# Kernel tuning notes

Measured on AMD Instinct MI355X. Metric: run time of the kernel, lower is better.

## Reference

```python
import jax, jax.numpy as jnp
import numpy as np

B, T, C, H = 4, 2048, 1024, 16
D = C // H  # head_size = 64


def setup_inputs() -> dict:
    key = jax.random.key(0)
    k1, k2, k3 = jax.random.split(key, 3)
    x = jax.random.normal(k1, (B, T, C), dtype=jnp.float32)
    w_qkv = jax.random.normal(k2, (C, 3 * C), dtype=jnp.float32) * (C ** -0.5)
    b_qkv = jnp.zeros((3 * C,), dtype=jnp.float32)
    w_proj = jax.random.normal(k3, (C, C), dtype=jnp.float32) * (C ** -0.5)
    b_proj = jnp.zeros((C,), dtype=jnp.float32)
    return {"x": x, "w_qkv": w_qkv, "b_qkv": b_qkv, "w_proj": w_proj, "b_proj": b_proj}


def reference(x, w_qkv, b_qkv, w_proj, b_proj):
    b, t, c = x.shape
    qkv = x @ w_qkv + b_qkv                      # [B,T,3C]
    q, k, v = jnp.split(qkv, 3, axis=-1)
    # [B,T,C] -> [B,H,T,D]
    q = q.reshape(b, t, H, D).transpose(0, 2, 1, 3)
    k = k.reshape(b, t, H, D).transpose(0, 2, 1, 3)
    v = v.reshape(b, t, H, D).transpose(0, 2, 1, 3)
    attn = jnp.einsum('bhqd,bhkd->bhqk', q, k) * (D ** -0.5)
    causal = jnp.tril(jnp.ones((t, t), dtype=bool))
    attn = jnp.where(causal[None, None], attn, -jnp.inf)
    attn = jax.nn.softmax(attn, axis=-1)
    # dropout: eval mode (identity)
    out = jnp.einsum('bhqk,bhkd->bhqd', attn, v)
    out = out.transpose(0, 2, 1, 3).reshape(b, t, c)
    return out @ w_proj + b_proj
```

## Files before the change

### kernel.cpp

```cpp
#include <hip/hip_runtime.h>

#define B_ 4
#define T_ 2048
#define C_ 1024
#define H_ 16
#define D_ 64

typedef __attribute__((ext_vector_type(8))) short short8;
typedef __attribute__((ext_vector_type(4))) float f32x4;

__device__ inline unsigned short f2bf(float f) {
    union { float f; unsigned u; } v; v.f = f;
    unsigned r = v.u + 0x7fffu + ((v.u >> 16) & 1u);
    return (unsigned short)(r >> 16);
}

__device__ inline unsigned int pk_bf16(float a, float b) {
#if __has_builtin(__builtin_amdgcn_cvt_pk_bf16_f32)
    typedef __attribute__((ext_vector_type(2))) __bf16 bf16x2;
    bf16x2 v = __builtin_amdgcn_cvt_pk_bf16_f32(a, b);
    return __builtin_bit_cast(unsigned int, v);
#else
    return (unsigned)f2bf(a) | ((unsigned)f2bf(b) << 16);
#endif
}

__device__ inline float dpp_max16(float x) {
    int t;
    t = __builtin_amdgcn_update_dpp(0, __builtin_bit_cast(int, x), 0xB1, 0xF, 0xF, true);
    x = fmaxf(x, __builtin_bit_cast(float, t));
    t = __builtin_amdgcn_update_dpp(0, __builtin_bit_cast(int, x), 0x4E, 0xF, 0xF, true);
    x = fmaxf(x, __builtin_bit_cast(float, t));
    t = __builtin_amdgcn_update_dpp(0, __builtin_bit_cast(int, x), 0x141, 0xF, 0xF, true);
    x = fmaxf(x, __builtin_bit_cast(float, t));
    t = __builtin_amdgcn_update_dpp(0, __builtin_bit_cast(int, x), 0x140, 0xF, 0xF, true);
    x = fmaxf(x, __builtin_bit_cast(float, t));
    return x;
}

__device__ inline void async_ld16(const void* g, void* lds) {
    __builtin_amdgcn_global_load_lds(
        (const __attribute__((address_space(1))) unsigned int*)g,
        (__attribute__((address_space(3))) unsigned int*)lds, 16, 0, 0);
}

__global__ __launch_bounds__(256) void prep_all(
    const float* __restrict__ x, const float* __restrict__ w_qkv,
    const float* __restrict__ w_proj,
    unsigned short* __restrict__ xb, unsigned short* __restrict__ wqkvT,
    unsigned short* __restrict__ wprojT)
{
    const int bid = blockIdx.x;
    if (bid < 8192) {
        int i = (bid * 256 + threadIdx.x) * 4;
        float4 v = *(const float4*)(x + i);
        uint2 o;
        o.x = pk_bf16(v.x, v.y);
        o.y = pk_bf16(v.z, v.w);
        *(uint2*)(xb + i) = o;
        return;
    }
    __shared__ float tile[32][33];
    const int tt = bid - 8192;
    int bx = tt & 127;
    const int by = tt >> 7;
    const float* src; unsigned short* dst; int Cc;
    if (bx < 96) { src = w_qkv;  dst = wqkvT;  Cc = 3072; }
    else         { src = w_proj; dst = wprojT; Cc = 1024; bx -= 96; }
    const int tx = threadIdx.x & 31, ty = threadIdx.x >> 5;
    #pragma unroll
    for (int r = 0; r < 32; r += 8)
        tile[ty + r][tx] = src[(size_t)(by*32 + ty + r) * Cc + bx*32 + tx];
    __syncthreads();
    #pragma unroll
    for (int r = 0; r < 32; r += 8)
        dst[(size_t)(bx*32 + ty + r) * 1024 + by*32 + tx] = f2bf(tile[tx][ty + r]);
}

__global__ __launch_bounds__(256) void gemm_qkv(
    const unsigned short* __restrict__ A,
    const unsigned short* __restrict__ BT,
    const float* __restrict__ bias,
    unsigned short* __restrict__ qb, unsigned short* __restrict__ kb,
    unsigned short* __restrict__ vtb)
{
    __shared__ unsigned short As0[128 * 32], As1[128 * 32];
    __shared__ unsigned short Bs0[128 * 32], Bs1[128 * 32];
    const int tid = threadIdx.x;
    const int wave = tid >> 6, lane = tid & 63;
    const int wm = wave >> 1, wn = wave & 1;
    const int l15 = lane & 15, lq = lane >> 4;
    const int m0 = blockIdx.y * 128, n0 = blockIdx.x * 128;
    const int srow = tid >> 2, sg = tid & 3;
    const int sel = n0 >> 10;

    f32x4 acc[4][4] = {};

    for (int k0 = 0; k0 < 1024; k0 += 64) {
        #pragma unroll
        for (int r = 0; r < 2; ++r) {
            const size_t ra = (size_t)(m0 + r*64 + srow) * 1024 + k0 + sg*8;
            const size_t rb = (size_t)(n0 + r*64 + srow) * 1024 + k0 + sg*8;
            async_ld16(A  + ra,      (char*)As0 + r*4096 + wave*1024);
            async_ld16(A  + ra + 32, (char*)As1 + r*4096 + wave*1024);
            async_ld16(BT + rb,      (char*)Bs0 + r*4096 + wave*1024);
            async_ld16(BT + rb + 32, (char*)Bs1 + r*4096 + wave*1024);
        }
        __syncthreads();
        #pragma unroll
        for (int ks = 0; ks < 2; ++ks) {
            const unsigned short* Asx = ks ? As1 : As0;
            const unsigned short* Bsx = ks ? Bs1 : Bs0;
            short8 af[4], bf[4];
            #pragma unroll
            for (int i = 0; i < 4; ++i) {
                af[i] = *(const short8*)&Asx[(wm*64 + i*16 + l15) * 32 + lq*8];
                bf[i] = *(const short8*)&Bsx[(wn*64 + i*16 + l15) * 32 + lq*8];
            }
            if (sel < 2) {
                #pragma unroll
                for (int mi = 0; mi < 4; ++mi)
                    #pragma unroll
                    for (int ni = 0; ni < 4; ++ni)
                        acc[mi][ni] = __builtin_amdgcn_mfma_f32_16x16x32_bf16(
                            bf[ni], af[mi], acc[mi][ni], 0, 0, 0);
            } else {
                #pragma unroll
                for (int mi = 0; mi < 4; ++mi)
                    #pragma unroll
                    for (int ni = 0; ni < 4; ++ni)
                        acc[mi][ni] = __builtin_amdgcn_mfma_f32_16x16x32_bf16(
                            af[mi], bf[ni], acc[mi][ni], 0, 0, 0);
            }
        }
        __syncthreads();
    }

    if (sel < 2) {
        const float qs = (sel == 0) ? 0.180336880f : 1.0f;
        unsigned short* dst = (sel == 0) ? qb : kb;
        #pragma unroll
        for (int mi = 0; mi < 4; ++mi) {
            const int t = m0 + wm*64 + mi*16 + l15;
            const int bb = t >> 11, tt = t & 2047;
            #pragma unroll
            for (int ni = 0; ni < 4; ++ni) {
                const int nb = n0 + wn*64 + ni*16 + lq*4;
                const int hh = (nb >> 6) & 15, d0 = nb & 63;
                float4 bv = *(const float4*)(bias + nb);
                float v0 = (acc[mi][ni][0] + bv.x) * qs;
                float v1 = (acc[mi][ni][1] + bv.y) * qs;
                float v2 = (acc[mi][ni][2] + bv.z) * qs;
                float v3 = (acc[mi][ni][3] + bv.w) * qs;
                uint2 pk; pk.x = pk_bf16(v0, v1); pk.y = pk_bf16(v2, v3);
                *(uint2*)(dst + ((size_t)(bb*16 + hh)*2048 + tt)*64 + d0) = pk;
            }
        }
    } else {
        #pragma unroll
        for (int mi = 0; mi < 4; ++mi) {
            const int t0 = m0 + wm*64 + mi*16 + lq*4;
            const int bb = t0 >> 11, tt = t0 & 2047;
            #pragma unroll
            for (int ni = 0; ni < 4; ++ni) {
                const int n = n0 + wn*64 + ni*16 + l15;
                const int hh = (n >> 6) & 15, d = n & 63;
                const float bs = bias[n];
                uint2 pk;
                pk.x = pk_bf16(acc[mi][ni][0] + bs, acc[mi][ni][1] + bs);
                pk.y = pk_bf16(acc[mi][ni][2] + bs, acc[mi][ni][3] + bs);
                *(uint2*)(vtb + ((size_t)(bb*16 + hh)*64 + d)*2048 + tt) = pk;
            }
        }
    }
}

__global__ __launch_bounds__(256) void gemm_proj(
    const unsigned short* __restrict__ A,
    const unsigned short* __restrict__ BT,
    const float* __restrict__ bias,
    float* __restrict__ out)
{
    __shared__ unsigned short As0[128 * 32], As1[128 * 32];
    __shared__ unsigned short Bs0[128 * 32], Bs1[128 * 32];
    const int tid = threadIdx.x;
    const int wave = tid >> 6, lane = tid & 63;
    const int wm = wave >> 1, wn = wave & 1;
    const int l15 = lane & 15, lq = lane >> 4;
    const int m0 = blockIdx.y * 128, n0 = blockIdx.x * 128;
    const int srow = tid >> 2, sg = tid & 3;

    f32x4 acc[4][4] = {};

    for (int k0 = 0; k0 < 1024; k0 += 64) {
        #pragma unroll
        for (int r = 0; r < 2; ++r) {
            const size_t ra = (size_t)(m0 + r*64 + srow) * 1024 + k0 + sg*8;
            const size_t rb = (size_t)(n0 + r*64 + srow) * 1024 + k0 + sg*8;
            async_ld16(A  + ra,      (char*)As0 + r*4096 + wave*1024);
            async_ld16(A  + ra + 32, (char*)As1 + r*4096 + wave*1024);
            async_ld16(BT + rb,      (char*)Bs0 + r*4096 + wave*1024);
            async_ld16(BT + rb + 32, (char*)Bs1 + r*4096 + wave*1024);
        }
        __syncthreads();
        #pragma unroll
        for (int ks = 0; ks < 2; ++ks) {
            const unsigned short* Asx = ks ? As1 : As0;
            const unsigned short* Bsx = ks ? Bs1 : Bs0;
            short8 af[4], bf[4];
            #pragma unroll
            for (int i = 0; i < 4; ++i) {
                af[i] = *(const short8*)&Asx[(wm*64 + i*16 + l15) * 32 + lq*8];
                bf[i] = *(const short8*)&Bsx[(wn*64 + i*16 + l15) * 32 + lq*8];
            }
            #pragma unroll
            for (int mi = 0; mi < 4; ++mi)
                #pragma unroll
                for (int ni = 0; ni < 4; ++ni)
                    acc[mi][ni] = __builtin_amdgcn_mfma_f32_16x16x32_bf16(
                        bf[ni], af[mi], acc[mi][ni], 0, 0, 0);
        }
        __syncthreads();
    }

    #pragma unroll
    for (int mi = 0; mi < 4; ++mi) {
        const int m = m0 + wm*64 + mi*16 + l15;
        #pragma unroll
        for (int ni = 0; ni < 4; ++ni) {
            const int nb = n0 + wn*64 + ni*16 + lq*4;
            float4 bv = *(const float4*)(bias + nb);
            float4 o;
            o.x = acc[mi][ni][0] + bv.x;
            o.y = acc[mi][ni][1] + bv.y;
            o.z = acc[mi][ni][2] + bv.z;
            o.w = acc[mi][ni][3] + bv.w;
            *(float4*)(out + (size_t)m * 1024 + nb) = o;
        }
    }
}

__global__ __launch_bounds__(256, 5) void attn_mfma(
    const unsigned short* __restrict__ qb,
    const unsigned short* __restrict__ kb,
    const unsigned short* __restrict__ vtb,
    unsigned short* __restrict__ ab)
{
    __shared__ unsigned short Ks[64][72];
    __shared__ unsigned short Vt[80][72];
    __shared__ unsigned short Ps[64][72];

    const int tid  = threadIdx.x;
    const int wave = tid >> 6, lane = tid & 63;
    const int l15  = lane & 15, lq = lane >> 4;
    const int linear = blockIdx.x;
    const int xc  = linear & 7;
    const int idx = linear >> 3;
    const int bh  = xc * 8 + (idx & 7);
    const int qblk = 31 - (idx >> 3);
    const int q0 = qblk * 64;
    const int b = bh >> 4, h = bh & 15;
    const size_t base = (size_t)bh * 2048 * 64;

    for (int i = tid; i < 16 * 72; i += 256) {
        int r = i / 72, cc = i - r * 72;
        Vt[64 + r][cc] = (r == 0) ? (unsigned short)0x3F80 : (unsigned short)0;
    }
    #pragma unroll
    for (int i = 0; i < 2; ++i) {
        int slot = tid + 256 * i;
        int row = slot >> 3, g = slot & 7;
        *(uint4*)&Ps[row][g*8] = *(const uint4*)(qb + base + (size_t)(q0 + row)*64 + g*8);
    }
    __syncthreads();
    short8 qf[2];
    qf[0] = *(const short8*)&Ps[wave*16 + l15][lq*8];
    qf[1] = *(const short8*)&Ps[wave*16 + l15][32 + lq*8];

    f32x4 o[4] = {}, lac = {};
    float mrow[4] = {-1e30f, -1e30f, -1e30f, -1e30f};

    for (int j0 = 0; j0 <= q0; j0 += 64) {
        __syncthreads();
        #pragma unroll
        for (int i = 0; i < 2; ++i) {
            int slot = tid + 256 * i;
            int row = slot >> 3, g = slot & 7;
            *(uint4*)&Ks[row][g*8] = *(const uint4*)(kb  + base + (size_t)(j0 + row)*64 + g*8);
            *(uint4*)&Vt[row][g*8] = *(const uint4*)(vtb + base + (size_t)row*2048 + j0 + g*8);
        }
        __syncthreads();

        f32x4 s[4] = {};
        #pragma unroll
        for (int ks = 0; ks < 2; ++ks)
            #pragma unroll
            for (int ni = 0; ni < 4; ++ni) {
                short8 kf = *(const short8*)&Ks[ni*16 + l15][ks*32 + lq*8];
                s[ni] = __builtin_amdgcn_mfma_f32_16x16x32_bf16(qf[ks], kf, s[ni], 0, 0, 0);
            }

        if (j0 == q0) {
            #pragma unroll
            for (int ni = 0; ni < 4; ++ni) {
                int kc = ni*16 + l15;
                #pragma unroll
                for (int r = 0; r < 4; ++r) {
                    int qr = wave*16 + lq*4 + r;
                    if (kc > qr) s[ni][r] = -1e30f;
                }
            }
        }

        float al[4];
        #pragma unroll
        for (int r = 0; r < 4; ++r) {
            float mx = fmaxf(fmaxf(s[0][r], s[1][r]), fmaxf(s[2][r], s[3][r]));
            mx = dpp_max16(mx);
            float mnew = fmaxf(mrow[r], mx);
            al[r] = __builtin_amdgcn_exp2f(mrow[r] - mnew);
            mrow[r] = mnew;
        }
        #pragma unroll
        for (int r = 0; r < 4; ++r) {
            float p0 = __builtin_amdgcn_exp2f(s[0][r] - mrow[r]);
            float p1 = __builtin_amdgcn_exp2f(s[1][r] - mrow[r]);
            float p2 = __builtin_amdgcn_exp2f(s[2][r] - mrow[r]);
            float p3 = __builtin_amdgcn_exp2f(s[3][r] - mrow[r]);
            unsigned pa = pk_bf16(p0, p1), pb = pk_bf16(p2, p3);
            const int row = wave*16 + lq*4 + r;
            Ps[row][l15]      = (unsigned short)pa;
            Ps[row][16 + l15] = (unsigned short)(pa >> 16);
            Ps[row][32 + l15] = (unsigned short)pb;
            Ps[row][48 + l15] = (unsigned short)(pb >> 16);
            o[0][r] *= al[r]; o[1][r] *= al[r];
            o[2][r] *= al[r]; o[3][r] *= al[r];
            lac[r] *= al[r];
        }

        #pragma unroll
        for (int ks = 0; ks < 2; ++ks) {
            short8 pf = *(const short8*)&Ps[wave*16 + l15][ks*32 + lq*8];
            #pragma unroll
            for (int ni = 0; ni < 4; ++ni) {
                short8 vf = *(const short8*)&Vt[ni*16 + l15][ks*32 + lq*8];
                o[ni] = __builtin_amdgcn_mfma_f32_16x16x32_bf16(pf, vf, o[ni], 0, 0, 0);
            }
            short8 vl = *(const short8*)&Vt[64 + l15][ks*32 + lq*8];
            lac = __builtin_amdgcn_mfma_f32_16x16x32_bf16(pf, vl, lac, 0, 0, 0);
        }
    }

    #pragma unroll
    for (int r = 0; r < 4; ++r) {
        float l = __shfl(lac[r], (lane & 48));
        float linv = __builtin_amdgcn_rcpf(l);
        int m = b*2048 + q0 + wave*16 + lq*4 + r;
        unsigned pa = pk_bf16(o[0][r]*linv, o[1][r]*linv);
        unsigned pb = pk_bf16(o[2][r]*linv, o[3][r]*linv);
        unsigned short* p = ab + (size_t)m*1024 + h*64;
        p[l15]      = (unsigned short)pa;
        p[16 + l15] = (unsigned short)(pa >> 16);
        p[32 + l15] = (unsigned short)pb;
        p[48 + l15] = (unsigned short)(pb >> 16);
    }
}

extern "C" void kernel_launch(void* const* d_in, const int* in_sizes, int n_in,
                              void* d_out, int out_size, void* d_ws, size_t ws_size,
                              hipStream_t stream) {
    const float* x      = (const float*)d_in[0];
    const float* w_qkv  = (const float*)d_in[1];
    const float* b_qkv  = (const float*)d_in[2];
    const float* w_proj = (const float*)d_in[3];
    const float* b_proj = (const float*)d_in[4];
    float* out = (float*)d_out;

    unsigned short* xb     = (unsigned short*)d_ws;
    unsigned short* wqkvT  = xb + 8388608;
    unsigned short* wprojT = wqkvT + 3145728;
    unsigned short* qbuf   = wprojT + 1048576;
    unsigned short* kbuf   = qbuf + 8388608;
    unsigned short* vtbuf  = kbuf + 8388608;
    unsigned short* abuf   = vtbuf + 8388608;

    prep_all<<<12288, 256, 0, stream>>>(x, w_qkv, w_proj, xb, wqkvT, wprojT);
    gemm_qkv<<<dim3(24, 64), 256, 0, stream>>>(xb, wqkvT, b_qkv, qbuf, kbuf, vtbuf);
    attn_mfma<<<2048, 256, 0, stream>>>(qbuf, kbuf, vtbuf, abuf);
    gemm_proj<<<dim3(8, 64), 256, 0, stream>>>(abuf, wprojT, b_proj, out);
}
```

Baseline: 266.4 us.

## Split attention KV range across waves with async swizzled LDS staging

Restructures attention so each wave processes a strided subset of 64-key tiles for the whole 64-query block, then reduces the partial outputs and row sums across waves through LDS at the end. It computes S transposed (K as the A operand) and permutes the V^T layout in the QKV GEMM epilogue, so the probabilities feed the PV MFMA straight from registers with no P round trip through LDS. K and V tiles are loaded per wave with global_load_lds into XOR-swizzled buffers, using vmcnt waits to overlap loads with compute instead of block barriers. The online running max is removed and exp2 is applied to raw scores, which saves the max reductions and rescaling but can overflow if scores are large. The larger per-block LDS footprint lowers occupancy.

```diff
diff --git a/kernel.cpp b/kernel.cpp
--- a/kernel.cpp
+++ b/kernel.cpp
@@ -23,19 +23,6 @@
 #else
     return (unsigned)f2bf(a) | ((unsigned)f2bf(b) << 16);
 #endif
-}
-
-__device__ inline float dpp_max16(float x) {
-    int t;
-    t = __builtin_amdgcn_update_dpp(0, __builtin_bit_cast(int, x), 0xB1, 0xF, 0xF, true);
-    x = fmaxf(x, __builtin_bit_cast(float, t));
-    t = __builtin_amdgcn_update_dpp(0, __builtin_bit_cast(int, x), 0x4E, 0xF, 0xF, true);
-    x = fmaxf(x, __builtin_bit_cast(float, t));
-    t = __builtin_amdgcn_update_dpp(0, __builtin_bit_cast(int, x), 0x141, 0xF, 0xF, true);
-    x = fmaxf(x, __builtin_bit_cast(float, t));
-    t = __builtin_amdgcn_update_dpp(0, __builtin_bit_cast(int, x), 0x140, 0xF, 0xF, true);
-    x = fmaxf(x, __builtin_bit_cast(float, t));
-    return x;
 }
 
 __device__ inline void async_ld16(const void* g, void* lds) {
@@ -161,6 +148,8 @@
         for (int mi = 0; mi < 4; ++mi) {
             const int t0 = m0 + wm*64 + mi*16 + lq*4;
             const int bb = t0 >> 11, tt = t0 & 2047;
+            const int tl = tt & 63;
+            const int tp = (tt & ~63) | (tl & 32) | ((tl & 12) << 1) | ((tl & 16) >> 2);
             #pragma unroll
             for (int ni = 0; ni < 4; ++ni) {
                 const int n = n0 + wn*64 + ni*16 + l15;
@@ -169,7 +158,7 @@
                 uint2 pk;
                 pk.x = pk_bf16(acc[mi][ni][0] + bs, acc[mi][ni][1] + bs);
                 pk.y = pk_bf16(acc[mi][ni][2] + bs, acc[mi][ni][3] + bs);
-                *(uint2*)(vtb + ((size_t)(bb*16 + hh)*64 + d)*2048 + tt) = pk;
+                *(uint2*)(vtb + ((size_t)(bb*16 + hh)*64 + d)*2048 + tp) = pk;
             }
         }
     }
@@ -240,16 +229,13 @@
     }
 }
 
-__global__ __launch_bounds__(256, 5) void attn_mfma(
+__global__ __launch_bounds__(256, 2) void attn_mfma(
     const unsigned short* __restrict__ qb,
     const unsigned short* __restrict__ kb,
     const unsigned short* __restrict__ vtb,
     unsigned short* __restrict__ ab)
 {
-    __shared__ unsigned short Ks[64][72];
-    __shared__ unsigned short Vt[80][72];
-    __shared__ unsigned short Ps[64][72];
-
+    extern __shared__ unsigned char smem[];
     const int tid  = threadIdx.x;
     const int wave = tid >> 6, lane = tid & 63;
     const int l15  = lane & 15, lq = lane >> 4;
@@ -262,107 +248,157 @@
     const int b = bh >> 4, h = bh & 15;
     const size_t base = (size_t)bh * 2048 * 64;
 
-    for (int i = tid; i < 16 * 72; i += 256) {
-        int r = i / 72, cc = i - r * 72;
-        Vt[64 + r][cc] = (r == 0) ? (unsigned short)0x3F80 : (unsigned short)0;
-    }
-    #pragma unroll
-    for (int i = 0; i < 2; ++i) {
-        int slot = tid + 256 * i;
-        int row = slot >> 3, g = slot & 7;
-        *(uint4*)&Ps[row][g*8] = *(const uint4*)(qb + base + (size_t)(q0 + row)*64 + g*8);
+    unsigned short* Kw = (unsigned short*)(smem + wave * 16384);
+    unsigned short* Vw = Kw + 4096;
+
+    const int row8 = lane >> 3;
+    const int chx8 = ((lane & 7) ^ row8) * 8;
+
+#define STAGE_K(J0) do { _Pragma("unroll") for (int op = 0; op < 8; ++op) \
+    async_ld16(kb + base + (size_t)((J0) + op*8 + row8)*64 + chx8, \
+               (char*)Kw + op*1024); } while (0)
+#define STAGE_V(J0) do { _Pragma("unroll") for (int op = 0; op < 8; ++op) \
+    async_ld16(vtb + base + (size_t)(op*8 + row8)*2048 + (J0) + chx8, \
+               (char*)Vw + op*1024); } while (0)
+
+    short8 qf[2][4];
+    #pragma unroll
+    for (int ks = 0; ks < 2; ++ks)
+        #pragma unroll
+        for (int nq = 0; nq < 4; ++nq)
+            qf[ks][nq] = *(const short8*)(qb + base
+                + (size_t)(q0 + nq*16 + l15)*64 + ks*32 + lq*8);
+
+    f32x4 o[4][4] = {};
+    float lacc[4] = {0.f, 0.f, 0.f, 0.f};
+
+    const int jfirst = wave * 64;
+    const int nt = (qblk >= wave) ? ((qblk - wave) >> 2) + 1 : 0;
+
+    if (nt > 0) { STAGE_K(jfirst); STAGE_V(jfirst); }
+
+    for (int i = 0; i < nt; ++i) {
+        const int j0 = jfirst + i * 256;
+        const bool more = (i + 1 < nt);
+
+        asm volatile("s_waitcnt vmcnt(8)" ::: "memory");
+
+        short8 kf0[4], kf1[4];
+        #pragma unroll
+        for (int ni = 0; ni < 4; ++ni) {
+            const unsigned short* kr = Kw + (ni*16 + l15) * 64;
+            kf0[ni] = *(const short8*)(kr + (((0*4 + lq) ^ (l15 & 7)) << 3));
+            kf1[ni] = *(const short8*)(kr + (((1*4 + lq) ^ (l15 & 7)) << 3));
+        }
+        f32x4 s[4][4] = {};
+        #pragma unroll
+        for (int ni = 0; ni < 4; ++ni)
+            #pragma unroll
+            for (int nq = 0; nq < 4; ++nq) {
+                s[ni][nq] = __builtin_amdgcn_mfma_f32_16x16x32_bf16(
+                    kf0[ni], qf[0][nq], s[ni][nq], 0, 0, 0);
+                s[ni][nq] = __builtin_amdgcn_mfma_f32_16x16x32_bf16(
+                    kf1[ni], qf[1][nq], s[ni][nq], 0, 0, 0);
+            }
+        asm volatile("s_waitcnt lgkmcnt(0)" ::: "memory");
+        if (more) STAGE_K(j0 + 256);
+
+        if (j0 == q0) {
+            #pragma unroll
+            for (int ni = 0; ni < 4; ++ni)
+                #pragma unroll
+                for (int nq = 0; nq < 4; ++nq)
+                    #pragma unroll
+                    for (int r = 0; r < 4; ++r)
+                        if (ni*16 + lq*4 + r > nq*16 + l15)
+                            s[ni][nq][r] = -1e30f;
+        }
+
+        short8 pf[2][4];
+        #pragma unroll
+        for (int c = 0; c < 2; ++c)
+            #pragma unroll
+            for (int nq = 0; nq < 4; ++nq) {
+                float p0 = __builtin_amdgcn_exp2f(s[2*c  ][nq][0]);
+                float p1 = __builtin_amdgcn_exp2f(s[2*c  ][nq][1]);
+                float p2 = __builtin_amdgcn_exp2f(s[2*c  ][nq][2]);
+                float p3 = __builtin_amdgcn_exp2f(s[2*c  ][nq][3]);
+                float p4 = __builtin_amdgcn_exp2f(s[2*c+1][nq][0]);
+                float p5 = __builtin_amdgcn_exp2f(s[2*c+1][nq][1]);
+                float p6 = __builtin_amdgcn_exp2f(s[2*c+1][nq][2]);
+                float p7 = __builtin_amdgcn_exp2f(s[2*c+1][nq][3]);
+                lacc[nq] += ((p0 + p1) + (p2 + p3)) + ((p4 + p5) + (p6 + p7));
+                uint4 pu;
+                pu.x = pk_bf16(p0, p1); pu.y = pk_bf16(p2, p3);
+                pu.z = pk_bf16(p4, p5); pu.w = pk_bf16(p6, p7);
+                pf[c][nq] = __builtin_bit_cast(short8, pu);
+            }
+
+        if (more) asm volatile("s_waitcnt vmcnt(8)" ::: "memory");
+        else      asm volatile("s_waitcnt vmcnt(0)" ::: "memory");
+
+        #pragma unroll
+        for (int c = 0; c < 2; ++c) {
+            short8 vf[4];
+            #pragma unroll
+            for (int nd = 0; nd < 4; ++nd)
+                vf[nd] = *(const short8*)(Vw + (nd*16 + l15) * 64
+                    + (((c*4 + lq) ^ (l15 & 7)) << 3));
+            #pragma unroll
+            for (int nq = 0; nq < 4; ++nq)
+                #pragma unroll
+                for (int nd = 0; nd < 4; ++nd)
+                    o[nq][nd] = __builtin_amdgcn_mfma_f32_16x16x32_bf16(
+                        pf[c][nq], vf[nd], o[nq][nd], 0, 0, 0);
+        }
+        asm volatile("s_waitcnt lgkmcnt(0)" ::: "memory");
+        if (more) STAGE_V(j0 + 256);
+    }
+#undef STAGE_K
+#undef STAGE_V
+
+    #pragma unroll
+    for (int nq = 0; nq < 4; ++nq) {
+        float t = lacc[nq];
+        t += __shfl_xor(t, 16);
+        t += __shfl_xor(t, 32);
+        if (lq == 0) ((float*)Kw)[nq*16 + l15] = t;
     }
     __syncthreads();
-    short8 qf[2];
-    qf[0] = *(const short8*)&Ps[wave*16 + l15][lq*8];
-    qf[1] = *(const short8*)&Ps[wave*16 + l15][32 + lq*8];
-
-    f32x4 o[4] = {}, lac = {};
-    float mrow[4] = {-1e30f, -1e30f, -1e30f, -1e30f};
-
-    for (int j0 = 0; j0 <= q0; j0 += 64) {
-        __syncthreads();
-        #pragma unroll
-        for (int i = 0; i < 2; ++i) {
-            int slot = tid + 256 * i;
-            int row = slot >> 3, g = slot & 7;
-            *(uint4*)&Ks[row][g*8] = *(const uint4*)(kb  + base + (size_t)(j0 + row)*64 + g*8);
-            *(uint4*)&Vt[row][g*8] = *(const uint4*)(vtb + base + (size_t)row*2048 + j0 + g*8);
-        }
-        __syncthreads();
-
-        f32x4 s[4] = {};
-        #pragma unroll
-        for (int ks = 0; ks < 2; ++ks)
-            #pragma unroll
-            for (int ni = 0; ni < 4; ++ni) {
-                short8 kf = *(const short8*)&Ks[ni*16 + l15][ks*32 + lq*8];
-                s[ni] = __builtin_amdgcn_mfma_f32_16x16x32_bf16(qf[ks], kf, s[ni], 0, 0, 0);
-            }
-
-        if (j0 == q0) {
-            #pragma unroll
-            for (int ni = 0; ni < 4; ++ni) {
-                int kc = ni*16 + l15;
-                #pragma unroll
-                for (int r = 0; r < 4; ++r) {
-                    int qr = wave*16 + lq*4 + r;
-                    if (kc > qr) s[ni][r] = -1e30f;
-                }
-            }
-        }
-
-        float al[4];
+    const int qg = wave, d = lane;
+    f32x4 linv4[4];
+    #pragma unroll
+    for (int j = 0; j < 4; ++j) {
+        f32x4 lsum = {};
+        #pragma unroll
+        for (int w2 = 0; w2 < 4; ++w2)
+            lsum += *(const f32x4*)((const float*)(smem + w2*16384) + qg*16 + j*4);
+        #pragma unroll
+        for (int r = 0; r < 4; ++r)
+            linv4[j][r] = __builtin_amdgcn_rcpf(lsum[r]);
+    }
+    __syncthreads();
+    #pragma unroll
+    for (int nq = 0; nq < 4; ++nq)
+        #pragma unroll
+        for (int nd = 0; nd < 4; ++nd) {
+            const int row = nd*16 + l15;
+            const int col = (nq*16 + lq*4 + 4*l15) & 63;
+            *(f32x4*)((float*)Kw + row*64 + col) = o[nq][nd];
+        }
+    __syncthreads();
+    #pragma unroll
+    for (int j = 0; j < 4; ++j) {
+        const int colb = (qg*16 + j*4 + 4*(d & 15)) & 63;
+        f32x4 acc = {};
+        #pragma unroll
+        for (int w2 = 0; w2 < 4; ++w2)
+            acc += *(const f32x4*)((const float*)(smem + w2*16384) + d*64 + colb);
         #pragma unroll
         for (int r = 0; r < 4; ++r) {
-            float mx = fmaxf(fmaxf(s[0][r], s[1][r]), fmaxf(s[2][r], s[3][r]));
-            mx = dpp_max16(mx);
-            float mnew = fmaxf(mrow[r], mx);
-            al[r] = __builtin_amdgcn_exp2f(mrow[r] - mnew);
-            mrow[r] = mnew;
-        }
-        #pragma unroll
-        for (int r = 0; r < 4; ++r) {
-            float p0 = __builtin_amdgcn_exp2f(s[0][r] - mrow[r]);
-            float p1 = __builtin_amdgcn_exp2f(s[1][r] - mrow[r]);
-            float p2 = __builtin_amdgcn_exp2f(s[2][r] - mrow[r]);
-            float p3 = __builtin_amdgcn_exp2f(s[3][r] - mrow[r]);
-            unsigned pa = pk_bf16(p0, p1), pb = pk_bf16(p2, p3);
-            const int row = wave*16 + lq*4 + r;
-            Ps[row][l15]      = (unsigned short)pa;
-            Ps[row][16 + l15] = (unsigned short)(pa >> 16);
-            Ps[row][32 + l15] = (unsigned short)pb;
-            Ps[row][48 + l15] = (unsigned short)(pb >> 16);
-            o[0][r] *= al[r]; o[1][r] *= al[r];
-            o[2][r] *= al[r]; o[3][r] *= al[r];
-            lac[r] *= al[r];
-        }
-
-        #pragma unroll
-        for (int ks = 0; ks < 2; ++ks) {
-            short8 pf = *(const short8*)&Ps[wave*16 + l15][ks*32 + lq*8];
-            #pragma unroll
-            for (int ni = 0; ni < 4; ++ni) {
-                short8 vf = *(const short8*)&Vt[ni*16 + l15][ks*32 + lq*8];
-                o[ni] = __builtin_amdgcn_mfma_f32_16x16x32_bf16(pf, vf, o[ni], 0, 0, 0);
-            }
-            short8 vl = *(const short8*)&Vt[64 + l15][ks*32 + lq*8];
-            lac = __builtin_amdgcn_mfma_f32_16x16x32_bf16(pf, vl, lac, 0, 0, 0);
-        }
-    }
-
-    #pragma unroll
-    for (int r = 0; r < 4; ++r) {
-        float l = __shfl(lac[r], (lane & 48));
-        float linv = __builtin_amdgcn_rcpf(l);
-        int m = b*2048 + q0 + wave*16 + lq*4 + r;
-        unsigned pa = pk_bf16(o[0][r]*linv, o[1][r]*linv);
-        unsigned pb = pk_bf16(o[2][r]*linv, o[3][r]*linv);
-        unsigned short* p = ab + (size_t)m*1024 + h*64;
-        p[l15]      = (unsigned short)pa;
-        p[16 + l15] = (unsigned short)(pa >> 16);
-        p[32 + l15] = (unsigned short)pb;
-        p[48 + l15] = (unsigned short)(pb >> 16);
+            const int q = qg*16 + j*4 + r;
+            ab[(size_t)(b*2048 + q0 + q)*1024 + h*64 + d] = f2bf(acc[r] * linv4[j][r]);
+        }
     }
 }
 
@@ -386,6 +422,6 @@
 
     prep_all<<<12288, 256, 0, stream>>>(x, w_qkv, w_proj, xb, wqkvT, wprojT);
     gemm_qkv<<<dim3(24, 64), 256, 0, stream>>>(xb, wqkvT, b_qkv, qbuf, kbuf, vtbuf);
-    attn_mfma<<<2048, 256, 0, stream>>>(qbuf, kbuf, vtbuf, abuf);
+    attn_mfma<<<2048, 256, 65536, stream>>>(qbuf, kbuf, vtbuf, abuf);
     gemm_proj<<<dim3(8, 64), 256, 0, stream>>>(abuf, wprojT, b_proj, out);
 }
```

Result: faster. 247.1 us (-7.2%).
